# Kernel optimization log

Measured on AMD Instinct MI355X. Metric: run time of the kernel, lower is better.

## Reference

```python
import jax, jax.numpy as jnp
import numpy as np

N = 100000   # nodes
G = 128      # graphs for mean pool


def gcn_conv(x, edge_index, W, b, num_nodes):
    # PyG GCNConv (default): x' = D^-1/2 (A+I) D^-1/2 (x W) + b
    x = x @ W
    src, dst = edge_index[0], edge_index[1]
    loop = jnp.arange(num_nodes)
    src = jnp.concatenate([src, loop])
    dst = jnp.concatenate([dst, loop])
    ones = jnp.ones(src.shape[0], x.dtype)
    deg = jax.ops.segment_sum(ones, dst, num_segments=num_nodes)
    dinv = jnp.where(deg > 0, jax.lax.rsqrt(deg), 0.0)
    norm = dinv[src] * dinv[dst]            # [E+N]
    msg = x[src] * norm[:, None]            # gather + scale
    out = jax.ops.segment_sum(msg, dst, num_segments=num_nodes)  # scatter-add
    return out + b


def setup_inputs() -> dict:
    key = jax.random.key(0)
    ks = jax.random.split(key, 5)
    x = jax.random.normal(ks[0], (N, 128), jnp.float32)
    edge_index = jax.random.randint(ks[1], (2, 1600000), 0, N)
    batch = jnp.sort(jax.random.randint(ks[2], (N,), 0, G))
    W1 = jax.random.normal(ks[3], (128, 64), jnp.float32) / np.sqrt(128.0)
    b1 = jnp.zeros((64,), jnp.float32)
    W2 = jax.random.normal(ks[4], (64, 64), jnp.float32) / np.sqrt(64.0)
    b2 = jnp.zeros((64,), jnp.float32)
    return {"x": x, "edge_index": edge_index, "batch": batch,
            "W1": W1, "b1": b1, "W2": W2, "b2": b2}


def reference(x, edge_index, batch, W1, b1, W2, b2):
    h = gcn_conv(x, edge_index, W1, b1, N)
    h = jax.nn.relu(h)  # dropout is identity in eval mode
    h = gcn_conv(h, edge_index, W2, b2, N)
    # global_mean_pool over graph ids
    s = jax.ops.segment_sum(h, batch, num_segments=G)
    cnt = jax.ops.segment_sum(jnp.ones((N,), h.dtype), batch, num_segments=G)
    return s / jnp.maximum(cnt, 1.0)[:, None]   # [G, hidden2]
```

## Files before the change

kernel.cpp:

```cpp
#include <hip/hip_runtime.h>
#include <hip/hip_fp16.h>

#define SLOTS 64
#define DEGSTRIDE 16

typedef _Float16 half8 __attribute__((ext_vector_type(8)));
typedef float f32x4 __attribute__((ext_vector_type(4)));

__global__ __launch_bounds__(256) void fill_pad(const int* __restrict__ src,
                                                const int* __restrict__ dst, int E, int N,
                                                int* __restrict__ degp,
                                                int* __restrict__ colpad, int chunks) {
  int range = blockIdx.x & 7;
  int chunk = blockIdx.x >> 3;
  int per = (N + 7) >> 3;
  int lo = range * per, hi = min(N, lo + per);
  int e0 = (int)((long long)chunk * E / chunks);
  int e1 = (int)((long long)(chunk + 1) * E / chunks);
  for (int e = e0 + (int)threadIdx.x; e < e1; e += 256) {
    int d = dst[e];
    if (d >= lo && d < hi) {
      int p = atomicAdd(&degp[(size_t)d * DEGSTRIDE], 1);
      if (p < SLOTS) colpad[(size_t)d * SLOTS + p] = src[e];
    }
  }
}

__global__ __launch_bounds__(256) void calc_dinv(const int* __restrict__ degp,
                                                 float* __restrict__ dinv,
                                                 int* __restrict__ degc, int N) {
  int i = blockIdx.x * 256 + threadIdx.x;
  if (i < N) {
    int d = degp[(size_t)i * DEGSTRIDE];
    dinv[i] = rsqrtf((float)(d + 1));
    degc[i] = min(d, SLOTS);
  }
}

template <int K, typename Tin>
__global__ __launch_bounds__(256) void gemm_mfma(const Tin* __restrict__ in,
                                                 const float* __restrict__ W,
                                                 const float* __restrict__ dinv,
                                                 __half* __restrict__ out,
                                                 int N, int tiles) {
  constexpr int LDK = K + 8;
  __shared__ __align__(16) _Float16 Wt[64][LDK];
  int t = threadIdx.x;
  for (int j = t; j < K * 64; j += 256) {
    int k = j >> 6, c = j & 63;
    Wt[c][k] = (_Float16)W[j];
  }
  __syncthreads();
  int wave = t >> 6, lane = t & 63;
  int arow = lane & 15, kgrp = lane >> 4;
  constexpr int KK = K / 32;

  for (int tile = blockIdx.x; tile < tiles; tile += gridDim.x) {
    int row0 = tile * 64;
    int row = row0 + wave * 16 + arow;
    half8 af[KK];
    if (row < N) {
#pragma unroll
      for (int kk = 0; kk < KK; ++kk) {
        if constexpr (sizeof(Tin) == 4) {
          const float4* p = (const float4*)&in[(size_t)row * K + kk * 32 + kgrp * 8];
          float4 v0 = p[0], v1 = p[1];
          half8 h;
          h[0] = (_Float16)v0.x; h[1] = (_Float16)v0.y;
          h[2] = (_Float16)v0.z; h[3] = (_Float16)v0.w;
          h[4] = (_Float16)v1.x; h[5] = (_Float16)v1.y;
          h[6] = (_Float16)v1.z; h[7] = (_Float16)v1.w;
          af[kk] = h;
        } else {
          af[kk] = *(const half8*)&in[(size_t)row * K + kk * 32 + kgrp * 8];
        }
      }
    } else {
#pragma unroll
      for (int kk = 0; kk < KK; ++kk) af[kk] = (half8)((_Float16)0.f);
    }
    f32x4 acc[4];
#pragma unroll
    for (int ct = 0; ct < 4; ++ct) acc[ct] = (f32x4)(0.f);
#pragma unroll
    for (int kk = 0; kk < KK; ++kk) {
#pragma unroll
      for (int ct = 0; ct < 4; ++ct) {
        half8 b = *(const half8*)&Wt[ct * 16 + arow][kk * 32 + kgrp * 8];
        acc[ct] = __builtin_amdgcn_mfma_f32_16x16x32_f16(af[kk], b, acc[ct], 0, 0, 0);
      }
    }
    int rbase = row0 + wave * 16 + kgrp * 4;
#pragma unroll
    for (int r = 0; r < 4; ++r) {
      int rr = rbase + r;
      if (rr < N) {
        float s = dinv[rr];
#pragma unroll
        for (int ct = 0; ct < 4; ++ct)
          out[(size_t)rr * 64 + ct * 16 + arow] = __float2half(acc[ct][r] * s);
      }
    }
  }
}

__global__ __launch_bounds__(256) void aggregate(const __half* __restrict__ g,
                                                 const int* __restrict__ degc,
                                                 const int* __restrict__ colpad,
                                                 const float* __restrict__ dinv,
                                                 const float* __restrict__ bias,
                                                 const int* __restrict__ batch,
                                                 __half* __restrict__ out,
                                                 float* __restrict__ poolsum,
                                                 float* __restrict__ poolcnt,
                                                 int N, int mode) {
  int lane = threadIdx.x & 63;
  int wave = blockIdx.x * 4 + (threadIdx.x >> 6);
  int nwaves = gridDim.x * 4;
  int per = (N + nwaves - 1) / nwaves;
  int n0 = wave * per, n1 = min(N, n0 + per);
  if (n0 >= n1) return;
  float b = bias[lane];
  int cur = mode ? batch[n0] : 0;
  float pacc = 0.f, pcnt = 0.f;
  int deg = degc[n0];
  int nb = colpad[(size_t)n0 * SLOTS + lane];
  for (int node = n0; node < n1; ++node) {
    int nxt = (node + 1 < n1) ? node + 1 : node;
    int dn = degc[nxt];
    int nbn = colpad[(size_t)nxt * SLOTS + lane];
    float a0 = __half2float(g[(size_t)node * 64 + lane]);
    float a1 = 0.f, a2 = 0.f, a3 = 0.f;
    float a4 = 0.f, a5 = 0.f, a6 = 0.f, a7 = 0.f;
    int j = 0;
    for (; j + 7 < deg; j += 8) {
      int s0 = __shfl(nb, j, 64);
      int s1 = __shfl(nb, j + 1, 64);
      int s2 = __shfl(nb, j + 2, 64);
      int s3 = __shfl(nb, j + 3, 64);
      int s4 = __shfl(nb, j + 4, 64);
      int s5 = __shfl(nb, j + 5, 64);
      int s6 = __shfl(nb, j + 6, 64);
      int s7 = __shfl(nb, j + 7, 64);
      a0 += __half2float(g[(size_t)s0 * 64 + lane]);
      a1 += __half2float(g[(size_t)s1 * 64 + lane]);
      a2 += __half2float(g[(size_t)s2 * 64 + lane]);
      a3 += __half2float(g[(size_t)s3 * 64 + lane]);
      a4 += __half2float(g[(size_t)s4 * 64 + lane]);
      a5 += __half2float(g[(size_t)s5 * 64 + lane]);
      a6 += __half2float(g[(size_t)s6 * 64 + lane]);
      a7 += __half2float(g[(size_t)s7 * 64 + lane]);
    }
    for (; j + 3 < deg; j += 4) {
      int s0 = __shfl(nb, j, 64);
      int s1 = __shfl(nb, j + 1, 64);
      int s2 = __shfl(nb, j + 2, 64);
      int s3 = __shfl(nb, j + 3, 64);
      a0 += __half2float(g[(size_t)s0 * 64 + lane]);
      a1 += __half2float(g[(size_t)s1 * 64 + lane]);
      a2 += __half2float(g[(size_t)s2 * 64 + lane]);
      a3 += __half2float(g[(size_t)s3 * 64 + lane]);
    }
    for (; j < deg; ++j) a0 += __half2float(g[(size_t)__shfl(nb, j, 64) * 64 + lane]);
    float r = dinv[node] * (((a0 + a1) + (a2 + a3)) + ((a4 + a5) + (a6 + a7))) + b;
    deg = dn;
    nb = nbn;
    if (mode == 0) {
      out[(size_t)node * 64 + lane] = __float2half(fmaxf(r, 0.f));
    } else {
      int bg = batch[node];
      if (bg != cur) {
        atomicAdd(&poolsum[cur * 64 + lane], pacc);
        if (lane == 0) atomicAdd(&poolcnt[cur], pcnt);
        pacc = 0.f; pcnt = 0.f; cur = bg;
      }
      pacc += r; pcnt += 1.f;
    }
  }
  if (mode) {
    atomicAdd(&poolsum[cur * 64 + lane], pacc);
    if (lane == 0) atomicAdd(&poolcnt[cur], pcnt);
  }
}

__global__ __launch_bounds__(256) void finalize(const float* __restrict__ poolsum,
                                                const float* __restrict__ poolcnt,
                                                float* __restrict__ out, int Gn) {
  int i = blockIdx.x * 256 + threadIdx.x;
  if (i < Gn * 64) {
    float c = poolcnt[i >> 6];
    out[i] = poolsum[i] / fmaxf(c, 1.f);
  }
}

extern "C" void kernel_launch(void* const* d_in, const int* in_sizes, int n_in,
                              void* d_out, int out_size, void* d_ws, size_t ws_size,
                              hipStream_t stream) {
  const float* x   = (const float*)d_in[0];
  const int* ei    = (const int*)d_in[1];
  const int* batch = (const int*)d_in[2];
  const float* W1  = (const float*)d_in[3];
  const float* b1  = (const float*)d_in[4];
  const float* W2  = (const float*)d_in[5];
  const float* b2  = (const float*)d_in[6];
  float* out = (float*)d_out;

  int N  = in_sizes[2];
  int E  = in_sizes[1] / 2;
  int Gn = out_size / 64;

  char* ws = (char*)d_ws;
  size_t off = 0;
  auto alloc = [&](size_t bytes) -> void* {
    void* p = ws + off;
    off = (off + bytes + 255) & ~(size_t)255;
    return p;
  };
  float* poolsum = (float*)alloc(4ull * Gn * 64);
  float* poolcnt = (float*)alloc(4ull * Gn);
  size_t zero_bytes = off;
  int* colpad    = (int*)alloc(4ull * (size_t)N * SLOTS);
  float* dinv    = (float*)alloc(4ull * N);
  int* degc      = (int*)alloc(4ull * N);
  __half* gbuf   = (__half*)alloc(2ull * (size_t)N * 64);
  __half* ybuf   = (__half*)alloc(2ull * (size_t)N * 64);
  int* degp = (int*)gbuf;
  (void)ws_size; (void)n_in;

  hipMemsetAsync(poolsum, 0, zero_bytes, stream);
  hipMemsetAsync(degp, 0, 4ull * (size_t)N * DEGSTRIDE, stream);

  const int* srcv = ei;
  const int* dstv = ei + E;
  int tiles64 = (N + 63) / 64;

  fill_pad<<<8 * 256, 256, 0, stream>>>(srcv, dstv, E, N, degp, colpad, 256);
  calc_dinv<<<(N + 255) / 256, 256, 0, stream>>>(degp, dinv, degc, N);

  gemm_mfma<128, float><<<tiles64, 256, 0, stream>>>(x, W1, dinv, gbuf, N, tiles64);
  aggregate<<<2048, 256, 0, stream>>>(gbuf, degc, colpad, dinv, b1, batch, ybuf,
                                      nullptr, nullptr, N, 0);
  gemm_mfma<64, __half><<<tiles64, 256, 0, stream>>>(ybuf, W2, dinv, gbuf, N, tiles64);
  aggregate<<<2048, 256, 0, stream>>>(gbuf, degc, colpad, dinv, b2, batch, nullptr,
                                      poolsum, poolcnt, N, 1);
  finalize<<<(Gn * 64 + 255) / 256, 256, 0, stream>>>(poolsum, poolcnt, out, Gn);
}
```

Baseline: 309.8 us.

## Vectorize edge reads, software-pipeline GEMM tiles, widen aggregate unroll to 16

fill_pad now reads dst and src four edges at a time with int4 loads, and skips the src load when none of the four destinations fall in the block's node range. The GEMM switches to a persistent grid of 512 blocks and prefetches the next tile's A fragments into registers while the current tile computes. The aggregate loop gains a 16-way unrolled gather with 16 independent accumulators to keep more memory loads in flight. These changes aim to cut edge-scan bandwidth and latency stalls, at the cost of more register pressure and lower occupancy.

```diff
diff --git a/kernel.cpp b/kernel.cpp
--- a/kernel.cpp
+++ b/kernel.cpp
@@ -15,13 +15,43 @@
   int chunk = blockIdx.x >> 3;
   int per = (N + 7) >> 3;
   int lo = range * per, hi = min(N, lo + per);
-  int e0 = (int)((long long)chunk * E / chunks);
-  int e1 = (int)((long long)(chunk + 1) * E / chunks);
-  for (int e = e0 + (int)threadIdx.x; e < e1; e += 256) {
-    int d = dst[e];
-    if (d >= lo && d < hi) {
-      int p = atomicAdd(&degp[(size_t)d * DEGSTRIDE], 1);
-      if (p < SLOTS) colpad[(size_t)d * SLOTS + p] = src[e];
+  int W4 = (E + 3) >> 2;
+  int w0 = (int)((long long)chunk * W4 / chunks);
+  int w1 = (int)((long long)(chunk + 1) * W4 / chunks);
+  for (int w = w0 + (int)threadIdx.x; w < w1; w += 256) {
+    int e = w << 2;
+    int4 d4, s4;
+    if (e + 3 < E) {
+      d4 = *(const int4*)&dst[e];
+      bool m0 = (d4.x >= lo) & (d4.x < hi);
+      bool m1 = (d4.y >= lo) & (d4.y < hi);
+      bool m2 = (d4.z >= lo) & (d4.z < hi);
+      bool m3 = (d4.w >= lo) & (d4.w < hi);
+      if (!(m0 | m1 | m2 | m3)) continue;
+      s4 = *(const int4*)&src[e];
+    } else {
+      d4 = make_int4(-1, -1, -1, -1);
+      s4 = make_int4(0, 0, 0, 0);
+      if (e + 0 < E) { d4.x = dst[e + 0]; s4.x = src[e + 0]; }
+      if (e + 1 < E) { d4.y = dst[e + 1]; s4.y = src[e + 1]; }
+      if (e + 2 < E) { d4.z = dst[e + 2]; s4.z = src[e + 2]; }
+      if (e + 3 < E) { d4.w = dst[e + 3]; s4.w = src[e + 3]; }
+    }
+    if (d4.x >= lo && d4.x < hi) {
+      int p = atomicAdd(&degp[(size_t)d4.x * DEGSTRIDE], 1);
+      if (p < SLOTS) colpad[(size_t)d4.x * SLOTS + p] = s4.x;
+    }
+    if (d4.y >= lo && d4.y < hi) {
+      int p = atomicAdd(&degp[(size_t)d4.y * DEGSTRIDE], 1);
+      if (p < SLOTS) colpad[(size_t)d4.y * SLOTS + p] = s4.y;
+    }
+    if (d4.z >= lo && d4.z < hi) {
+      int p = atomicAdd(&degp[(size_t)d4.z * DEGSTRIDE], 1);
+      if (p < SLOTS) colpad[(size_t)d4.z * SLOTS + p] = s4.z;
+    }
+    if (d4.w >= lo && d4.w < hi) {
+      int p = atomicAdd(&degp[(size_t)d4.w * DEGSTRIDE], 1);
+      if (p < SLOTS) colpad[(size_t)d4.w * SLOTS + p] = s4.w;
     }
   }
 }
@@ -55,10 +85,8 @@
   int arow = lane & 15, kgrp = lane >> 4;
   constexpr int KK = K / 32;
 
-  for (int tile = blockIdx.x; tile < tiles; tile += gridDim.x) {
-    int row0 = tile * 64;
-    int row = row0 + wave * 16 + arow;
-    half8 af[KK];
+  auto load_af = [&](int tile, half8* af) {
+    int row = tile * 64 + wave * 16 + arow;
     if (row < N) {
 #pragma unroll
       for (int kk = 0; kk < KK; ++kk) {
@@ -79,6 +107,14 @@
 #pragma unroll
       for (int kk = 0; kk < KK; ++kk) af[kk] = (half8)((_Float16)0.f);
     }
+  };
+
+  half8 afA[KK], afB[KK];
+  int tile = blockIdx.x;
+  if (tile < tiles) load_af(tile, afA);
+  for (; tile < tiles; tile += gridDim.x) {
+    int nxt = tile + gridDim.x;
+    if (nxt < tiles) load_af(nxt, afB);
     f32x4 acc[4];
 #pragma unroll
     for (int ct = 0; ct < 4; ++ct) acc[ct] = (f32x4)(0.f);
@@ -87,10 +123,10 @@
 #pragma unroll
       for (int ct = 0; ct < 4; ++ct) {
         half8 b = *(const half8*)&Wt[ct * 16 + arow][kk * 32 + kgrp * 8];
-        acc[ct] = __builtin_amdgcn_mfma_f32_16x16x32_f16(af[kk], b, acc[ct], 0, 0, 0);
+        acc[ct] = __builtin_amdgcn_mfma_f32_16x16x32_f16(afA[kk], b, acc[ct], 0, 0, 0);
       }
     }
-    int rbase = row0 + wave * 16 + kgrp * 4;
+    int rbase = tile * 64 + wave * 16 + kgrp * 4;
 #pragma unroll
     for (int r = 0; r < 4; ++r) {
       int rr = rbase + r;
@@ -101,6 +137,8 @@
           out[(size_t)rr * 64 + ct * 16 + arow] = __float2half(acc[ct][r] * s);
       }
     }
+#pragma unroll
+    for (int kk = 0; kk < KK; ++kk) afA[kk] = afB[kk];
   }
 }
 
@@ -132,7 +170,43 @@
     float a0 = __half2float(g[(size_t)node * 64 + lane]);
     float a1 = 0.f, a2 = 0.f, a3 = 0.f;
     float a4 = 0.f, a5 = 0.f, a6 = 0.f, a7 = 0.f;
+    float a8 = 0.f, a9 = 0.f, aA = 0.f, aB = 0.f;
+    float aC = 0.f, aD = 0.f, aE = 0.f, aF = 0.f;
     int j = 0;
+    for (; j + 15 < deg; j += 16) {
+      int s0 = __shfl(nb, j, 64);
+      int s1 = __shfl(nb, j + 1, 64);
+      int s2 = __shfl(nb, j + 2, 64);
+      int s3 = __shfl(nb, j + 3, 64);
+      int s4 = __shfl(nb, j + 4, 64);
+      int s5 = __shfl(nb, j + 5, 64);
+      int s6 = __shfl(nb, j + 6, 64);
+      int s7 = __shfl(nb, j + 7, 64);
+      int s8 = __shfl(nb, j + 8, 64);
+      int s9 = __shfl(nb, j + 9, 64);
+      int sA = __shfl(nb, j + 10, 64);
+      int sB = __shfl(nb, j + 11, 64);
+      int sC = __shfl(nb, j + 12, 64);
+      int sD = __shfl(nb, j + 13, 64);
+      int sE = __shfl(nb, j + 14, 64);
+      int sF = __shfl(nb, j + 15, 64);
+      a0 += __half2float(g[(size_t)s0 * 64 + lane]);
+      a1 += __half2float(g[(size_t)s1 * 64 + lane]);
+      a2 += __half2float(g[(size_t)s2 * 64 + lane]);
+      a3 += __half2float(g[(size_t)s3 * 64 + lane]);
+      a4 += __half2float(g[(size_t)s4 * 64 + lane]);
+      a5 += __half2float(g[(size_t)s5 * 64 + lane]);
+      a6 += __half2float(g[(size_t)s6 * 64 + lane]);
+      a7 += __half2float(g[(size_t)s7 * 64 + lane]);
+      a8 += __half2float(g[(size_t)s8 * 64 + lane]);
+      a9 += __half2float(g[(size_t)s9 * 64 + lane]);
+      aA += __half2float(g[(size_t)sA * 64 + lane]);
+      aB += __half2float(g[(size_t)sB * 64 + lane]);
+      aC += __half2float(g[(size_t)sC * 64 + lane]);
+      aD += __half2float(g[(size_t)sD * 64 + lane]);
+      aE += __half2float(g[(size_t)sE * 64 + lane]);
+      aF += __half2float(g[(size_t)sF * 64 + lane]);
+    }
     for (; j + 7 < deg; j += 8) {
       int s0 = __shfl(nb, j, 64);
       int s1 = __shfl(nb, j + 1, 64);
@@ -162,7 +236,8 @@
       a3 += __half2float(g[(size_t)s3 * 64 + lane]);
     }
     for (; j < deg; ++j) a0 += __half2float(g[(size_t)__shfl(nb, j, 64) * 64 + lane]);
-    float r = dinv[node] * (((a0 + a1) + (a2 + a3)) + ((a4 + a5) + (a6 + a7))) + b;
+    float r = dinv[node] * ((((a0 + a1) + (a2 + a3)) + ((a4 + a5) + (a6 + a7))) +
+                            (((a8 + a9) + (aA + aB)) + ((aC + aD) + (aE + aF)))) + b;
     deg = dn;
     nb = nbn;
     if (mode == 0) {
@@ -237,10 +312,10 @@
   fill_pad<<<8 * 256, 256, 0, stream>>>(srcv, dstv, E, N, degp, colpad, 256);
   calc_dinv<<<(N + 255) / 256, 256, 0, stream>>>(degp, dinv, degc, N);
 
-  gemm_mfma<128, float><<<tiles64, 256, 0, stream>>>(x, W1, dinv, gbuf, N, tiles64);
+  gemm_mfma<128, float><<<512, 256, 0, stream>>>(x, W1, dinv, gbuf, N, tiles64);
   aggregate<<<2048, 256, 0, stream>>>(gbuf, degc, colpad, dinv, b1, batch, ybuf,
                                       nullptr, nullptr, N, 0);
-  gemm_mfma<64, __half><<<tiles64, 256, 0, stream>>>(ybuf, W2, dinv, gbuf, N, tiles64);
+  gemm_mfma<64, __half><<<512, 256, 0, stream>>>(ybuf, W2, dinv, gbuf, N, tiles64);
   aggregate<<<2048, 256, 0, stream>>>(gbuf, degc, colpad, dinv, b2, batch, nullptr,
                                       poolsum, poolcnt, N, 1);
   finalize<<<(Gn * 64 + 255) / 256, 256, 0, stream>>>(poolsum, poolcnt, out, Gn);
```

After: 350.5 us. 1.13x slower.
